# Optimization experiments

Measured on AMD Instinct MI355X. Metric: run time of the kernel, lower is better.

## Reference

```python
import jax, jax.numpy as jnp
import numpy as np
import math

B, T, C, H, L, V = 16, 512, 1024, 16, 4, 32000
D = C // H


def setup_inputs() -> dict:
    key = jax.random.key(0)
    ks = jax.random.split(key, 10)
    X = jax.random.randint(ks[0], (B, T), 0, V)
    S = jax.random.bernoulli(ks[1], 0.5, (B, T)).astype(jnp.int32)
    # I + S must equal 1 everywhere, else get_attn_mask fully masks a row -> NaN softmax
    I = (1 - S).astype(jnp.float32)
    s = 0.02
    emb_table = jax.random.normal(ks[2], (V + 1, C), jnp.float32) * s
    pos_emb = jax.random.normal(ks[3], (T, C), jnp.float32) * s
    qkv_w = jax.random.normal(ks[4], (L, 3 * C, C), jnp.float32) * s
    out_w = jax.random.normal(ks[5], (L, C, C), jnp.float32) * s
    ffn_w1 = jax.random.normal(ks[6], (L, C, C), jnp.float32) * s
    ffn_b1 = jnp.zeros((L, C), jnp.float32)
    ffn_w2 = jax.random.normal(ks[7], (L, C, C), jnp.float32) * s
    ffn_b2 = jnp.zeros((L, C), jnp.float32)
    return dict(X=X, I=I, S=S, emb_table=emb_table, pos_emb=pos_emb,
                qkv_w=qkv_w, out_w=out_w, ffn_w1=ffn_w1, ffn_b1=ffn_b1,
                ffn_w2=ffn_w2, ffn_b2=ffn_b2)


def _forward(X, I, S, emb_table, pos_emb, qkv_w, out_w, ffn_w1, ffn_b1, ffn_w2, ffn_b2):
    # token_to_embeddings: unobserved (S==0) tokens remapped to sentinel index V
    Xm = X * S + (1 - S) * V                      # [B,T]
    x = emb_table[Xm] + pos_emb[None]             # [B,T,C]
    # additive mask from outer product of validity flags m = I + S
    m = I + S.astype(I.dtype)                     # [B,T]
    prod = m[:, :, None] * m[:, None, :]          # [B,T,T]
    bias = jnp.where(prod == 1.0, 0.0, -jnp.inf)[:, None]  # [B,1,T,T]
    scale = 1.0 / math.sqrt(D)
    for i in range(L):
        wq, wk, wv = qkv_w[i, :C], qkv_w[i, C:2 * C], qkv_w[i, 2 * C:]
        q = (x @ wq.T).reshape(B, T, H, D)
        k = (x @ wk.T).reshape(B, T, H, D)
        v = (x @ wv.T).reshape(B, T, H, D)
        scores = jnp.einsum('bqhd,bkhd->bhqk', q * scale, k) + bias
        attn = jax.nn.softmax(scores, axis=-1)
        o = jnp.einsum('bhqk,bkhd->bqhd', attn, v).reshape(B, T, C)
        x = o @ out_w[i].T + x                    # out projection + residual
        h = jax.nn.relu(x @ ffn_w1[i].T + ffn_b1[i])
        x = x + (h @ ffn_w2[i].T + ffn_b2[i])
    # readout: bmm(x^T, I) -> [B,C]
    return jnp.einsum('btc,bt->bc', x, I)


def reference(X, I, S, emb_table, pos_emb, qkv_w, out_w, ffn_w1, ffn_b1, ffn_w2, ffn_b2):
    return _forward(X, I, S, emb_table, pos_emb, qkv_w, out_w,
                    ffn_w1, ffn_b1, ffn_w2, ffn_b2)
```

## Files before the change

kernel.cpp:

```cpp
#include <hip/hip_runtime.h>
#include <stdint.h>

#define LAYERS 4
#define BB 16
#define TT 512
#define CC 1024
#define HH 16
#define DD 64
#define VV 32000
#define MM (BB*TT)

typedef __attribute__((ext_vector_type(8))) short bf16x8;
typedef __attribute__((ext_vector_type(4))) float f32x4;
typedef __attribute__((ext_vector_type(16))) float f32x16;

__device__ __forceinline__ unsigned short f2b(float f) {
  union { float f; unsigned int u; } v; v.f = f;
  unsigned int r = v.u + 0x7FFFu + ((v.u >> 16) & 1u);
  return (unsigned short)(r >> 16);
}
__device__ __forceinline__ float blo(unsigned int u) {
  union { unsigned int x; float f; } v; v.x = u << 16; return v.f;
}
__device__ __forceinline__ float bhi(unsigned int u) {
  union { unsigned int x; float f; } v; v.x = u & 0xFFFF0000u; return v.f;
}
__device__ __forceinline__ uint32_t pkbf(float lo, float hi) {
  uint32_t d; asm("v_cvt_pk_bf16_f32 %0, %1, %2" : "=v"(d) : "v"(lo), "v"(hi)); return d;
}
__device__ __forceinline__ float ex2(float x) {
  float r; asm("v_exp_f32 %0, %1" : "=v"(r) : "v"(x)); return r;
}
__device__ __forceinline__ void gload16(const unsigned short* g, const unsigned short* lds) {
  __builtin_amdgcn_global_load_lds((const __attribute__((address_space(1))) void*)g,
                                   (__attribute__((address_space(3))) void*)lds, 16, 0, 0);
}

__global__ __launch_bounds__(256) void cvt_kernel(const float* __restrict__ src,
                                                  unsigned short* __restrict__ dst, int n4) {
  int i = blockIdx.x * 256 + threadIdx.x;
  if (i >= n4) return;
  float4 v = ((const float4*)src)[i];
  ushort4 o; o.x = f2b(v.x); o.y = f2b(v.y); o.z = f2b(v.z); o.w = f2b(v.w);
  ((ushort4*)dst)[i] = o;
}

__global__ __launch_bounds__(256) void embed_kernel(const int* __restrict__ X, const int* __restrict__ S,
    const float* __restrict__ emb, const float* __restrict__ pos,
    float* __restrict__ x, unsigned short* __restrict__ xb) {
  int bt = blockIdx.x; int tid = threadIdx.x;
  int t = bt & (TT - 1);
  int tok = S[bt] ? X[bt] : VV;
  float4 e = ((const float4*)(emb + (size_t)tok * CC))[tid];
  float4 p = ((const float4*)(pos + (size_t)t * CC))[tid];
  float4 r; r.x = e.x + p.x; r.y = e.y + p.y; r.z = e.z + p.z; r.w = e.w + p.w;
  ((float4*)(x + (size_t)bt * CC))[tid] = r;
  ushort4 ub; ub.x = f2b(r.x); ub.y = f2b(r.y); ub.z = f2b(r.z); ub.w = f2b(r.w);
  ((ushort4*)(xb + (size_t)bt * CC))[tid] = ub;
}

template<int EPI>
__global__ __launch_bounds__(512, 1) void gemm4_kernel(
    const unsigned short* __restrict__ A,
    const unsigned short* __restrict__ W,
    float* __restrict__ xres,
    unsigned short* __restrict__ outb,
    const float* __restrict__ bias,
    int N, int nbx) {
  extern __shared__ unsigned short lds[];
  const int K = 1024;
  const int tid = threadIdx.x;
  const int wv = tid >> 6, ln = tid & 63;
  const int g = ln >> 4, rr = ln & 15;
  const int wm = wv >> 1, wn = wv & 1;

  const int nwg = gridDim.x;
  const int bid = blockIdx.x;
  const int swz = (bid & 7) * (nwg >> 3) + (bid >> 3);
  const int by = swz / nbx, bx = swz - by * nbx;
  const int brow = by * 256, bcol = bx * 128;

  const unsigned short* asrc[4];
  const unsigned short* bsrc[2];
  #pragma unroll
  for (int rd = 0; rd < 4; ++rd) {
    int ch = rd * 512 + tid;
    int row = ch >> 3, c = (ch & 7) ^ (row & 7);
    asrc[rd] = A + (size_t)(brow + row) * K + c * 8;
  }
  #pragma unroll
  for (int rd = 0; rd < 2; ++rd) {
    int ch = rd * 512 + tid;
    int row = ch >> 3, c = (ch & 7) ^ (row & 7);
    bsrc[rd] = W + (size_t)(bcol + row) * K + c * 8;
  }

  auto stage = [&](int tile, int buf) {
    unsigned short* Ad = lds + buf * 24576 + wv * 512;
    unsigned short* Bd = lds + buf * 24576 + 16384 + wv * 512;
    int ko = tile * 64;
    #pragma unroll
    for (int rd = 0; rd < 4; ++rd) gload16(asrc[rd] + ko, Ad + rd * 4096);
    #pragma unroll
    for (int rd = 0; rd < 2; ++rd) gload16(bsrc[rd] + ko, Bd + rd * 4096);
  };

  f32x4 acc[4][4];
  #pragma unroll
  for (int i = 0; i < 4; ++i)
    #pragma unroll
    for (int j = 0; j < 4; ++j)
      acc[i][j] = (f32x4){0.f, 0.f, 0.f, 0.f};

  stage(0, 0);
  stage(1, 1);

  int bufc = 0;
  for (int t = 0; t < 16; ++t) {
    int bufn = bufc + 2; if (bufn >= 3) bufn -= 3;
    if (t < 14) {
      stage(t + 2, bufn);
      asm volatile("s_waitcnt vmcnt(12)" ::: "memory");
    } else if (t == 14) {
      asm volatile("s_waitcnt vmcnt(6)" ::: "memory");
    } else {
      asm volatile("s_waitcnt vmcnt(0)" ::: "memory");
    }
    __builtin_amdgcn_s_barrier();
    __builtin_amdgcn_sched_barrier(0);

    const unsigned short* Ab = lds + bufc * 24576;
    const unsigned short* Bb = Ab + 16384;
    bf16x8 av[2][4], bv[2][4];
    #pragma unroll
    for (int kk = 0; kk < 2; ++kk) {
      int chx = ((kk * 4 + g) ^ (rr & 7)) << 3;
      #pragma unroll
      for (int i = 0; i < 4; ++i) {
        av[kk][i] = *(const bf16x8*)(Ab + (wm * 64 + i * 16 + rr) * 64 + chx);
        bv[kk][i] = *(const bf16x8*)(Bb + (wn * 64 + i * 16 + rr) * 64 + chx);
      }
    }
    __builtin_amdgcn_s_setprio(1);
    #pragma unroll
    for (int kk = 0; kk < 2; ++kk)
      #pragma unroll
      for (int i = 0; i < 4; ++i)
        #pragma unroll
        for (int j = 0; j < 4; ++j)
          acc[i][j] = __builtin_amdgcn_mfma_f32_16x16x32_bf16(av[kk][i], bv[kk][j], acc[i][j], 0, 0, 0);
    __builtin_amdgcn_s_setprio(0);
    __builtin_amdgcn_sched_barrier(0);
    __builtin_amdgcn_s_barrier();
    bufc += 1; if (bufc == 3) bufc = 0;
  }

  #pragma unroll
  for (int i = 0; i < 4; ++i) {
    #pragma unroll
    for (int j = 0; j < 4; ++j) {
      #pragma unroll
      for (int q = 0; q < 4; ++q) {
        int rowg = brow + wm * 64 + i * 16 + g * 4 + q;
        int colg = bcol + wn * 64 + j * 16 + rr;
        size_t off = (size_t)rowg * N + colg;
        float vacc = acc[i][j][q];
        if (EPI == 0) {
          outb[off] = f2b(vacc);
        } else if (EPI == 1) {
          float nx = xres[off] + vacc;
          xres[off] = nx; outb[off] = f2b(nx);
        } else if (EPI == 2) {
          float hv = vacc + bias[colg];
          hv = hv > 0.f ? hv : 0.f;
          outb[off] = f2b(hv);
        } else {
          float nx = xres[off] + vacc + bias[colg];
          xres[off] = nx; outb[off] = f2b(nx);
        }
      }
    }
  }
}

template<int E>
__device__ __forceinline__ bf16x8 buildP(const f32x16& p) {
  uint32_t a = pkbf(p[E + 0], p[E + 1]);
  uint32_t b = pkbf(p[E + 4], p[E + 5]);
  uint32_t c = pkbf(p[E + 2], p[E + 3]);
  uint32_t d = pkbf(p[E + 6], p[E + 7]);
  asm("v_permlane32_swap_b32 %0, %1" : "+v"(a), "+v"(b));
  asm("v_permlane32_swap_b32 %0, %1" : "+v"(c), "+v"(d));
  union { uint32_t u[4]; bf16x8 v; } r;
  r.u[0] = a; r.u[1] = c; r.u[2] = b; r.u[3] = d;
  return r.v;
}

__global__ __launch_bounds__(256) void attn_kernel(const unsigned short* __restrict__ qkv,
                                                   unsigned short* __restrict__ ob) {
  __shared__ unsigned short Kl[64 * 64];
  __shared__ unsigned short Vt[64 * 64];
  const int tid = threadIdx.x;
  const int wv = tid >> 6, ln = tid & 63;
  const int lq = ln & 31, hi = ln >> 5;
  const int qt = blockIdx.x >> 8, bh = blockIdx.x & 255;
  const int b = bh >> 4, h = bh & 15;
  const int qrow = qt * 128 + wv * 32 + lq;
  const size_t rowQ = (size_t)(b * TT + qrow) * 3072 + h * 64;

  const float cs = 0.125f * 1.44269504f;
  bf16x8 qf[4];
  #pragma unroll
  for (int t = 0; t < 4; ++t) {
    uint4 u = *(const uint4*)(qkv + rowQ + t * 16 + hi * 8);
    uint32_t w[4] = {u.x, u.y, u.z, u.w};
    union { uint32_t u4[4]; bf16x8 v; } cv;
    #pragma unroll
    for (int j = 0; j < 4; ++j) cv.u4[j] = pkbf(blo(w[j]) * cs, bhi(w[j]) * cs);
    qf[t] = cv.v;
  }

  f32x16 o0 = {}, o1 = {};
  float mrun = -3.0e38f, lsum = 0.f;

  for (int kv0 = 0; kv0 < TT; kv0 += 64) {
    if (kv0) __syncthreads();
    #pragma unroll
    for (int r = 0; r < 2; ++r) {
      int ch = r * 256 + tid;
      int k = ch >> 3, cc = ch & 7;
      int sg = (k & 7) ^ (k >> 3);
      const unsigned short* gs = qkv + (size_t)(b * TT + kv0 + k) * 3072 + 1024 + h * 64 + ((cc ^ sg) << 3);
      gload16(gs, Kl + (size_t)(r * 256 + wv * 64) * 8);
    }
    {
      int cc = tid & 7, kp = tid >> 3;
      int k = kp * 2;
      const unsigned short* gv = qkv + (size_t)(b * TT + kv0 + k) * 3072 + 2048 + h * 64 + cc * 8;
      uint4 g1 = *(const uint4*)gv;
      uint4 g2 = *(const uint4*)(gv + 3072);
      uint32_t w1[4] = {g1.x, g1.y, g1.z, g1.w}, w2[4] = {g2.x, g2.y, g2.z, g2.w};
      #pragma unroll
      for (int j = 0; j < 8; ++j) {
        int d = cc * 8 + j;
        uint32_t dw = (j & 1) ? ((w1[j >> 1] >> 16) | (w2[j >> 1] & 0xFFFF0000u))
                              : ((w1[j >> 1] & 0xFFFFu) | (w2[j >> 1] << 16));
        int sg = (d & 7) ^ (d >> 3);
        *(uint32_t*)(Vt + d * 64 + (k ^ (sg << 3))) = dw;
      }
    }
    __syncthreads();

    f32x16 s0 = {}, s1 = {};
    #pragma unroll
    for (int t = 0; t < 4; ++t) {
      int r0 = lq, r1 = 32 + lq;
      bf16x8 a0 = *(const bf16x8*)(Kl + r0 * 64 + ((((t << 1) | hi) ^ ((r0 & 7) ^ (r0 >> 3))) << 3));
      bf16x8 a1 = *(const bf16x8*)(Kl + r1 * 64 + ((((t << 1) | hi) ^ ((r1 & 7) ^ (r1 >> 3))) << 3));
      s0 = __builtin_amdgcn_mfma_f32_32x32x16_bf16(a0, qf[t], s0, 0, 0, 0);
      s1 = __builtin_amdgcn_mfma_f32_32x32x16_bf16(a1, qf[t], s1, 0, 0, 0);
    }

    float mx = s0[0];
    #pragma unroll
    for (int r = 1; r < 16; ++r) mx = fmaxf(mx, s0[r]);
    #pragma unroll
    for (int r = 0; r < 16; ++r) mx = fmaxf(mx, s1[r]);
    mx = fmaxf(mx, __shfl_xor(mx, 32));
    float mnew = fmaxf(mrun, mx);
    float cf = ex2(mrun - mnew);
    mrun = mnew;
    lsum *= cf;
    #pragma unroll
    for (int r = 0; r < 16; ++r) { o0[r] *= cf; o1[r] *= cf; }
    #pragma unroll
    for (int r = 0; r < 16; ++r) {
      s0[r] = ex2(s0[r] - mnew);
      s1[r] = ex2(s1[r] - mnew);
      lsum += s0[r] + s1[r];
    }

    bf16x8 pf0 = buildP<0>(s0);
    bf16x8 pf1 = buildP<8>(s0);
    bf16x8 pf2 = buildP<0>(s1);
    bf16x8 pf3 = buildP<8>(s1);

    #pragma unroll
    for (int t = 0; t < 4; ++t) {
      bf16x8 pf = (t == 0) ? pf0 : (t == 1) ? pf1 : (t == 2) ? pf2 : pf3;
      int d0 = lq, d1 = 32 + lq;
      bf16x8 v0 = *(const bf16x8*)(Vt + d0 * 64 + ((((t << 1) | hi) ^ ((d0 & 7) ^ (d0 >> 3))) << 3));
      bf16x8 v1 = *(const bf16x8*)(Vt + d1 * 64 + ((((t << 1) | hi) ^ ((d1 & 7) ^ (d1 >> 3))) << 3));
      o0 = __builtin_amdgcn_mfma_f32_32x32x16_bf16(v0, pf, o0, 0, 0, 0);
      o1 = __builtin_amdgcn_mfma_f32_32x32x16_bf16(v1, pf, o1, 0, 0, 0);
    }
  }

  lsum += __shfl_xor(lsum, 32);
  float inv = 1.f / lsum;
  size_t orow = (size_t)(b * TT + qrow) * CC + h * 64;
  #pragma unroll
  for (int md = 0; md < 2; ++md) {
    #pragma unroll
    for (int rq = 0; rq < 4; ++rq) {
      int d0 = md * 32 + rq * 8 + hi * 4;
      float e0 = (md ? o1[rq * 4 + 0] : o0[rq * 4 + 0]) * inv;
      float e1 = (md ? o1[rq * 4 + 1] : o0[rq * 4 + 1]) * inv;
      float e2 = (md ? o1[rq * 4 + 2] : o0[rq * 4 + 2]) * inv;
      float e3 = (md ? o1[rq * 4 + 3] : o0[rq * 4 + 3]) * inv;
      uint2 st; st.x = pkbf(e0, e1); st.y = pkbf(e2, e3);
      *(uint2*)(ob + orow + d0) = st;
    }
  }
}

__global__ __launch_bounds__(256) void final_kernel(const float* __restrict__ x,
                                                    const float* __restrict__ I,
                                                    float* __restrict__ out) {
  int b = blockIdx.x >> 2;
  int c = ((blockIdx.x & 3) << 8) + threadIdx.x;
  float acc = 0.f;
  const float* xp = x + (size_t)b * TT * CC + c;
  const float* Ip = I + (size_t)b * TT;
  for (int t = 0; t < TT; ++t) acc = fmaf(xp[(size_t)t * CC], Ip[t], acc);
  out[b * CC + c] = acc;
}

extern "C" void kernel_launch(void* const* d_in, const int* in_sizes, int n_in,
                              void* d_out, int out_size, void* d_ws, size_t ws_size,
                              hipStream_t stream) {
  const int*   X      = (const int*)d_in[0];
  const float* I      = (const float*)d_in[1];
  const int*   S      = (const int*)d_in[2];
  const float* emb    = (const float*)d_in[3];
  const float* pos    = (const float*)d_in[4];
  const float* qkv_w  = (const float*)d_in[5];
  const float* out_w  = (const float*)d_in[6];
  const float* ffn_w1 = (const float*)d_in[7];
  const float* ffn_b1 = (const float*)d_in[8];
  const float* ffn_w2 = (const float*)d_in[9];
  const float* ffn_b2 = (const float*)d_in[10];
  float* out = (float*)d_out;

  char* ws = (char*)d_ws;
  size_t off = 0;
  auto walloc = [&](size_t bytes) { char* p = ws + off; off += (bytes + 255) & ~(size_t)255; return p; };
  unsigned short* wqkv = (unsigned short*)walloc((size_t)LAYERS * 3 * CC * CC * 2);
  unsigned short* wo   = (unsigned short*)walloc((size_t)LAYERS * CC * CC * 2);
  unsigned short* w1   = (unsigned short*)walloc((size_t)LAYERS * CC * CC * 2);
  unsigned short* w2   = (unsigned short*)walloc((size_t)LAYERS * CC * CC * 2);
  float*          x    = (float*)walloc((size_t)MM * CC * 4);
  unsigned short* xb   = (unsigned short*)walloc((size_t)MM * CC * 2);
  unsigned short* qkvb = (unsigned short*)walloc((size_t)MM * 3 * CC * 2);
  unsigned short* obuf = (unsigned short*)walloc((size_t)MM * CC * 2);
  unsigned short* hbuf = (unsigned short*)walloc((size_t)MM * CC * 2);
  if (off > ws_size) return;

  int n4;
  n4 = LAYERS * 3 * CC * CC / 4; cvt_kernel<<<(n4 + 255) / 256, 256, 0, stream>>>(qkv_w, wqkv, n4);
  n4 = LAYERS * CC * CC / 4;     cvt_kernel<<<(n4 + 255) / 256, 256, 0, stream>>>(out_w, wo, n4);
  n4 = LAYERS * CC * CC / 4;     cvt_kernel<<<(n4 + 255) / 256, 256, 0, stream>>>(ffn_w1, w1, n4);
  n4 = LAYERS * CC * CC / 4;     cvt_kernel<<<(n4 + 255) / 256, 256, 0, stream>>>(ffn_w2, w2, n4);

  embed_kernel<<<MM, 256, 0, stream>>>(X, S, emb, pos, x, xb);

  const size_t ldsB = 144 * 1024;
  for (int l = 0; l < LAYERS; ++l) {
    gemm4_kernel<0><<<(MM / 256) * (3 * CC / 128), 512, ldsB, stream>>>(
        xb, wqkv + (size_t)l * 3 * CC * CC, nullptr, qkvb, nullptr, 3 * CC, 3 * CC / 128);
    attn_kernel<<<4 * 256, 256, 0, stream>>>(qkvb, obuf);
    gemm4_kernel<1><<<(MM / 256) * (CC / 128), 512, ldsB, stream>>>(
        obuf, wo + (size_t)l * CC * CC, x, xb, nullptr, CC, CC / 128);
    gemm4_kernel<2><<<(MM / 256) * (CC / 128), 512, ldsB, stream>>>(
        xb, w1 + (size_t)l * CC * CC, nullptr, hbuf, ffn_b1 + l * CC, CC, CC / 128);
    gemm4_kernel<3><<<(MM / 256) * (CC / 128), 512, ldsB, stream>>>(
        hbuf, w2 + (size_t)l * CC * CC, x, xb, ffn_b2 + l * CC, CC, CC / 128);
  }

  final_kernel<<<BB * 4, 256, 0, stream>>>(x, I, out);
}
```

Baseline: 823.7 us.

## Split GEMM k-tile into two half-steps interleaving A/B prefetch with MFMA

Restructures the GEMM main loop so each 64-wide k tile is processed in two 32-wide halves. The A-tile global-to-LDS prefetch is issued in the first half and the B-tile prefetch in the second, each after that half's LDS fragment reads. The aim is to spread global load issue across the MFMA work and keep fewer fragment registers live. The cost is an extra barrier per k tile and changed waitcnt accounting, which could stall if the counts are off.

New measurement: 791.4 us. 1.04x faster.

```diff
diff --git a/kernel.cpp b/kernel.cpp
--- a/kernel.cpp
+++ b/kernel.cpp
@@ -60,7 +60,7 @@
 }
 
 template<int EPI>
-__global__ __launch_bounds__(512, 1) void gemm4_kernel(
+__global__ __launch_bounds__(512, 1) void gemm5_kernel(
     const unsigned short* __restrict__ A,
     const unsigned short* __restrict__ W,
     float* __restrict__ xres,
@@ -95,13 +95,16 @@
     bsrc[rd] = W + (size_t)(bcol + row) * K + c * 8;
   }
 
-  auto stage = [&](int tile, int buf) {
+  auto stageA = [&](int tile, int buf) {
     unsigned short* Ad = lds + buf * 24576 + wv * 512;
+    int ko = tile * 64;
+    #pragma unroll
+    for (int rd = 0; rd < 4; ++rd) gload16(asrc[rd] + ko, Ad + rd * 4096);
+  };
+  auto stageB = [&](int tile, int buf) {
     unsigned short* Bd = lds + buf * 24576 + 16384 + wv * 512;
     int ko = tile * 64;
     #pragma unroll
-    for (int rd = 0; rd < 4; ++rd) gload16(asrc[rd] + ko, Ad + rd * 4096);
-    #pragma unroll
     for (int rd = 0; rd < 2; ++rd) gload16(bsrc[rd] + ko, Bd + rd * 4096);
   };
 
@@ -112,46 +115,64 @@
     for (int j = 0; j < 4; ++j)
       acc[i][j] = (f32x4){0.f, 0.f, 0.f, 0.f};
 
-  stage(0, 0);
-  stage(1, 1);
+  stageA(0, 0); stageB(0, 0);
+  stageA(1, 1); stageB(1, 1);
+  asm volatile("s_waitcnt vmcnt(6)" ::: "memory");
+  __builtin_amdgcn_s_barrier();
 
   int bufc = 0;
   for (int t = 0; t < 16; ++t) {
     int bufn = bufc + 2; if (bufn >= 3) bufn -= 3;
-    if (t < 14) {
-      stage(t + 2, bufn);
-      asm volatile("s_waitcnt vmcnt(12)" ::: "memory");
-    } else if (t == 14) {
-      asm volatile("s_waitcnt vmcnt(6)" ::: "memory");
-    } else {
-      asm volatile("s_waitcnt vmcnt(0)" ::: "memory");
-    }
-    __builtin_amdgcn_s_barrier();
-    __builtin_amdgcn_sched_barrier(0);
-
     const unsigned short* Ab = lds + bufc * 24576;
     const unsigned short* Bb = Ab + 16384;
-    bf16x8 av[2][4], bv[2][4];
-    #pragma unroll
-    for (int kk = 0; kk < 2; ++kk) {
-      int chx = ((kk * 4 + g) ^ (rr & 7)) << 3;
-      #pragma unroll
-      for (int i = 0; i < 4; ++i) {
-        av[kk][i] = *(const bf16x8*)(Ab + (wm * 64 + i * 16 + rr) * 64 + chx);
-        bv[kk][i] = *(const bf16x8*)(Bb + (wn * 64 + i * 16 + rr) * 64 + chx);
-      }
-    }
-    __builtin_amdgcn_s_setprio(1);
-    #pragma unroll
-    for (int kk = 0; kk < 2; ++kk)
+
+    {
+      bf16x8 av[4], bv[4];
+      const int chx = ((0 * 4 + g) ^ (rr & 7)) << 3;
+      #pragma unroll
+      for (int i = 0; i < 4; ++i)
+        av[i] = *(const bf16x8*)(Ab + (wm * 64 + i * 16 + rr) * 64 + chx);
+      #pragma unroll
+      for (int j = 0; j < 4; ++j)
+        bv[j] = *(const bf16x8*)(Bb + (wn * 64 + j * 16 + rr) * 64 + chx);
+      if (t < 14) stageA(t + 2, bufn);
+      __builtin_amdgcn_sched_barrier(0);
+      __builtin_amdgcn_s_barrier();
+      __builtin_amdgcn_s_setprio(1);
       #pragma unroll
       for (int i = 0; i < 4; ++i)
         #pragma unroll
         for (int j = 0; j < 4; ++j)
-          acc[i][j] = __builtin_amdgcn_mfma_f32_16x16x32_bf16(av[kk][i], bv[kk][j], acc[i][j], 0, 0, 0);
-    __builtin_amdgcn_s_setprio(0);
-    __builtin_amdgcn_sched_barrier(0);
-    __builtin_amdgcn_s_barrier();
+          acc[i][j] = __builtin_amdgcn_mfma_f32_16x16x32_bf16(av[i], bv[j], acc[i][j], 0, 0, 0);
+      __builtin_amdgcn_s_setprio(0);
+      __builtin_amdgcn_sched_barrier(0);
+      __builtin_amdgcn_s_barrier();
+    }
+
+    {
+      bf16x8 av[4], bv[4];
+      const int chx = ((1 * 4 + g) ^ (rr & 7)) << 3;
+      #pragma unroll
+      for (int i = 0; i < 4; ++i)
+        av[i] = *(const bf16x8*)(Ab + (wm * 64 + i * 16 + rr) * 64 + chx);
+      #pragma unroll
+      for (int j = 0; j < 4; ++j)
+        bv[j] = *(const bf16x8*)(Bb + (wn * 64 + j * 16 + rr) * 64 + chx);
+      if (t < 14) stageB(t + 2, bufn);
+      __builtin_amdgcn_sched_barrier(0);
+      __builtin_amdgcn_s_barrier();
+      __builtin_amdgcn_s_setprio(1);
+      #pragma unroll
+      for (int i = 0; i < 4; ++i)
+        #pragma unroll
+        for (int j = 0; j < 4; ++j)
+          acc[i][j] = __builtin_amdgcn_mfma_f32_16x16x32_bf16(av[i], bv[j], acc[i][j], 0, 0, 0);
+      __builtin_amdgcn_s_setprio(0);
+      if (t < 14) { asm volatile("s_waitcnt vmcnt(6)" ::: "memory"); }
+      else if (t == 14) { asm volatile("s_waitcnt vmcnt(0)" ::: "memory"); }
+      __builtin_amdgcn_sched_barrier(0);
+      __builtin_amdgcn_s_barrier();
+    }
     bufc += 1; if (bufc == 3) bufc = 0;
   }
 
@@ -366,14 +387,14 @@
 
   const size_t ldsB = 144 * 1024;
   for (int l = 0; l < LAYERS; ++l) {
-    gemm4_kernel<0><<<(MM / 256) * (3 * CC / 128), 512, ldsB, stream>>>(
+    gemm5_kernel<0><<<(MM / 256) * (3 * CC / 128), 512, ldsB, stream>>>(
         xb, wqkv + (size_t)l * 3 * CC * CC, nullptr, qkvb, nullptr, 3 * CC, 3 * CC / 128);
     attn_kernel<<<4 * 256, 256, 0, stream>>>(qkvb, obuf);
-    gemm4_kernel<1><<<(MM / 256) * (CC / 128), 512, ldsB, stream>>>(
+    gemm5_kernel<1><<<(MM / 256) * (CC / 128), 512, ldsB, stream>>>(
         obuf, wo + (size_t)l * CC * CC, x, xb, nullptr, CC, CC / 128);
-    gemm4_kernel<2><<<(MM / 256) * (CC / 128), 512, ldsB, stream>>>(
+    gemm5_kernel<2><<<(MM / 256) * (CC / 128), 512, ldsB, stream>>>(
         xb, w1 + (size_t)l * CC * CC, nullptr, hbuf, ffn_b1 + l * CC, CC, CC / 128);
-    gemm4_kernel<3><<<(MM / 256) * (CC / 128), 512, ldsB, stream>>>(
+    gemm5_kernel<3><<<(MM / 256) * (CC / 128), 512, ldsB, stream>>>(
         hbuf, w2 + (size_t)l * CC * CC, x, xb, ffn_b2 + l * CC, CC, CC / 128);
   }
 
```

## Restructure GEMM to 256 threads, 2 blocks/CU, BK=32 with larger per-wave tiles

Applied to the files above, without the earlier changes.

The GEMM kernel moves from 512 threads with one block per CU to 256 threads with two blocks per CU. The K-tile drops from 64 to 32 (32 iterations), each wave now computes a 128x64 output tile with 8x4 accumulators, and LDS per block is halved so two blocks can share a CU. The aim is better latency hiding through two co-resident blocks and more MFMA work per LDS fragment load. The XOR swizzle on the LDS layout is removed, which may bring back bank conflicts, and the larger accumulator set raises register pressure.

After: 926.4 us. 12.5% more time.

```diff
diff --git a/kernel.cpp b/kernel.cpp
--- a/kernel.cpp
+++ b/kernel.cpp
@@ -60,7 +60,7 @@
 }
 
 template<int EPI>
-__global__ __launch_bounds__(512, 1) void gemm4_kernel(
+__global__ __launch_bounds__(256, 2) void gemm6_kernel(
     const unsigned short* __restrict__ A,
     const unsigned short* __restrict__ W,
     float* __restrict__ xres,
@@ -83,45 +83,41 @@
   const unsigned short* asrc[4];
   const unsigned short* bsrc[2];
   #pragma unroll
-  for (int rd = 0; rd < 4; ++rd) {
-    int ch = rd * 512 + tid;
-    int row = ch >> 3, c = (ch & 7) ^ (row & 7);
-    asrc[rd] = A + (size_t)(brow + row) * K + c * 8;
-  }
-  #pragma unroll
-  for (int rd = 0; rd < 2; ++rd) {
-    int ch = rd * 512 + tid;
-    int row = ch >> 3, c = (ch & 7) ^ (row & 7);
-    bsrc[rd] = W + (size_t)(bcol + row) * K + c * 8;
-  }
+  for (int rd = 0; rd < 4; ++rd)
+    asrc[rd] = A + (size_t)(brow + rd * 64 + (tid >> 2)) * K + (tid & 3) * 8;
+  #pragma unroll
+  for (int rd = 0; rd < 2; ++rd)
+    bsrc[rd] = W + (size_t)(bcol + rd * 64 + (tid >> 2)) * K + (tid & 3) * 8;
 
   auto stage = [&](int tile, int buf) {
-    unsigned short* Ad = lds + buf * 24576 + wv * 512;
-    unsigned short* Bd = lds + buf * 24576 + 16384 + wv * 512;
-    int ko = tile * 64;
-    #pragma unroll
-    for (int rd = 0; rd < 4; ++rd) gload16(asrc[rd] + ko, Ad + rd * 4096);
-    #pragma unroll
-    for (int rd = 0; rd < 2; ++rd) gload16(bsrc[rd] + ko, Bd + rd * 4096);
+    unsigned short* Ad = lds + buf * 12288 + wv * 512;
+    unsigned short* Bd = lds + buf * 12288 + 8192 + wv * 512;
+    int ko = tile * 32;
+    #pragma unroll
+    for (int rd = 0; rd < 4; ++rd) gload16(asrc[rd] + ko, Ad + rd * 2048);
+    #pragma unroll
+    for (int rd = 0; rd < 2; ++rd) gload16(bsrc[rd] + ko, Bd + rd * 2048);
   };
 
-  f32x4 acc[4][4];
-  #pragma unroll
-  for (int i = 0; i < 4; ++i)
+  f32x4 acc[8][4];
+  #pragma unroll
+  for (int i = 0; i < 8; ++i)
     #pragma unroll
     for (int j = 0; j < 4; ++j)
       acc[i][j] = (f32x4){0.f, 0.f, 0.f, 0.f};
 
   stage(0, 0);
   stage(1, 1);
+  asm volatile("s_waitcnt vmcnt(6)" ::: "memory");
+  __builtin_amdgcn_s_barrier();
 
   int bufc = 0;
-  for (int t = 0; t < 16; ++t) {
+  for (int t = 0; t < 32; ++t) {
     int bufn = bufc + 2; if (bufn >= 3) bufn -= 3;
-    if (t < 14) {
+    if (t < 30) {
       stage(t + 2, bufn);
       asm volatile("s_waitcnt vmcnt(12)" ::: "memory");
-    } else if (t == 14) {
+    } else if (t == 30) {
       asm volatile("s_waitcnt vmcnt(6)" ::: "memory");
     } else {
       asm volatile("s_waitcnt vmcnt(0)" ::: "memory");
@@ -129,26 +125,22 @@
     __builtin_amdgcn_s_barrier();
     __builtin_amdgcn_sched_barrier(0);
 
-    const unsigned short* Ab = lds + bufc * 24576;
-    const unsigned short* Bb = Ab + 16384;
-    bf16x8 av[2][4], bv[2][4];
-    #pragma unroll
-    for (int kk = 0; kk < 2; ++kk) {
-      int chx = ((kk * 4 + g) ^ (rr & 7)) << 3;
+    const unsigned short* Ab = lds + bufc * 12288;
+    const unsigned short* Bb = Ab + 8192;
+    bf16x8 av[8], bv[4];
+    #pragma unroll
+    for (int i = 0; i < 8; ++i)
+      av[i] = *(const bf16x8*)(Ab + (wm * 128 + i * 16 + rr) * 32 + g * 8);
+    #pragma unroll
+    for (int j = 0; j < 4; ++j)
+      bv[j] = *(const bf16x8*)(Bb + (wn * 64 + j * 16 + rr) * 32 + g * 8);
+
+    __builtin_amdgcn_s_setprio(1);
+    #pragma unroll
+    for (int i = 0; i < 8; ++i)
       #pragma unroll
-      for (int i = 0; i < 4; ++i) {
-        av[kk][i] = *(const bf16x8*)(Ab + (wm * 64 + i * 16 + rr) * 64 + chx);
-        bv[kk][i] = *(const bf16x8*)(Bb + (wn * 64 + i * 16 + rr) * 64 + chx);
-      }
-    }
-    __builtin_amdgcn_s_setprio(1);
-    #pragma unroll
-    for (int kk = 0; kk < 2; ++kk)
-      #pragma unroll
-      for (int i = 0; i < 4; ++i)
-        #pragma unroll
-        for (int j = 0; j < 4; ++j)
-          acc[i][j] = __builtin_amdgcn_mfma_f32_16x16x32_bf16(av[kk][i], bv[kk][j], acc[i][j], 0, 0, 0);
+      for (int j = 0; j < 4; ++j)
+        acc[i][j] = __builtin_amdgcn_mfma_f32_16x16x32_bf16(av[i], bv[j], acc[i][j], 0, 0, 0);
     __builtin_amdgcn_s_setprio(0);
     __builtin_amdgcn_sched_barrier(0);
     __builtin_amdgcn_s_barrier();
@@ -156,12 +148,12 @@
   }
 
   #pragma unroll
-  for (int i = 0; i < 4; ++i) {
+  for (int i = 0; i < 8; ++i) {
     #pragma unroll
     for (int j = 0; j < 4; ++j) {
       #pragma unroll
       for (int q = 0; q < 4; ++q) {
-        int rowg = brow + wm * 64 + i * 16 + g * 4 + q;
+        int rowg = brow + wm * 128 + i * 16 + g * 4 + q;
         int colg = bcol + wn * 64 + j * 16 + rr;
         size_t off = (size_t)rowg * N + colg;
         float vacc = acc[i][j][q];
@@ -364,16 +356,16 @@
 
   embed_kernel<<<MM, 256, 0, stream>>>(X, S, emb, pos, x, xb);
 
-  const size_t ldsB = 144 * 1024;
+  const size_t ldsB = 72 * 1024;
   for (int l = 0; l < LAYERS; ++l) {
-    gemm4_kernel<0><<<(MM / 256) * (3 * CC / 128), 512, ldsB, stream>>>(
+    gemm6_kernel<0><<<(MM / 256) * (3 * CC / 128), 256, ldsB, stream>>>(
         xb, wqkv + (size_t)l * 3 * CC * CC, nullptr, qkvb, nullptr, 3 * CC, 3 * CC / 128);
     attn_kernel<<<4 * 256, 256, 0, stream>>>(qkvb, obuf);
-    gemm4_kernel<1><<<(MM / 256) * (CC / 128), 512, ldsB, stream>>>(
+    gemm6_kernel<1><<<(MM / 256) * (CC / 128), 256, ldsB, stream>>>(
         obuf, wo + (size_t)l * CC * CC, x, xb, nullptr, CC, CC / 128);
-    gemm4_kernel<2><<<(MM / 256) * (CC / 128), 512, ldsB, stream>>>(
+    gemm6_kernel<2><<<(MM / 256) * (CC / 128), 256, ldsB, stream>>>(
         xb, w1 + (size_t)l * CC * CC, nullptr, hbuf, ffn_b1 + l * CC, CC, CC / 128);
-    gemm4_kernel<3><<<(MM / 256) * (CC / 128), 512, ldsB, stream>>>(
+    gemm6_kernel<3><<<(MM / 256) * (CC / 128), 256, ldsB, stream>>>(
         hbuf, w2 + (size_t)l * CC * CC, x, xb, ffn_b2 + l * CC, CC, CC / 128);
   }
 
```

## Use 4-wave GEMM with larger per-wave tiles and double-buffer attention K/V

Applied to the files above, without the earlier changes.

The GEMM now runs with 256 threads instead of 512, so each wave computes a 128x64 sub-tile. Each wave issues twice as many global-to-LDS loads, and the vmcnt waits are adjusted to match. The attention kernel gets double-buffered K and V^T tiles in shared memory: the next tile's K is staged and V is prefetched into registers while the current tile is computed. This replaces one of the two syncthreads per iteration with a single barrier, aiming to hide load latency. The trade-off is higher register pressure (32 accumulators per wave in the GEMM) and fewer waves available to hide latency.

Measured after the change: 934.0 us. +13.4%, slower.

```diff
diff --git a/kernel.cpp b/kernel.cpp
--- a/kernel.cpp
+++ b/kernel.cpp
@@ -60,7 +60,7 @@
 }
 
 template<int EPI>
-__global__ __launch_bounds__(512, 1) void gemm4_kernel(
+__global__ __launch_bounds__(256, 1) void gemm7_kernel(
     const unsigned short* __restrict__ A,
     const unsigned short* __restrict__ W,
     float* __restrict__ xres,
@@ -80,18 +80,18 @@
   const int by = swz / nbx, bx = swz - by * nbx;
   const int brow = by * 256, bcol = bx * 128;
 
-  const unsigned short* asrc[4];
-  const unsigned short* bsrc[2];
+  const unsigned short* asrc[8];
+  const unsigned short* bsrc[4];
+  #pragma unroll
+  for (int rd = 0; rd < 8; ++rd) {
+    int row = rd * 32 + (tid >> 3);
+    int c = (tid & 7) ^ (row & 7);
+    asrc[rd] = A + (size_t)(brow + row) * K + c * 8;
+  }
   #pragma unroll
   for (int rd = 0; rd < 4; ++rd) {
-    int ch = rd * 512 + tid;
-    int row = ch >> 3, c = (ch & 7) ^ (row & 7);
-    asrc[rd] = A + (size_t)(brow + row) * K + c * 8;
-  }
-  #pragma unroll
-  for (int rd = 0; rd < 2; ++rd) {
-    int ch = rd * 512 + tid;
-    int row = ch >> 3, c = (ch & 7) ^ (row & 7);
+    int row = rd * 32 + (tid >> 3);
+    int c = (tid & 7) ^ (row & 7);
     bsrc[rd] = W + (size_t)(bcol + row) * K + c * 8;
   }
 
@@ -100,29 +100,31 @@
     unsigned short* Bd = lds + buf * 24576 + 16384 + wv * 512;
     int ko = tile * 64;
     #pragma unroll
-    for (int rd = 0; rd < 4; ++rd) gload16(asrc[rd] + ko, Ad + rd * 4096);
-    #pragma unroll
-    for (int rd = 0; rd < 2; ++rd) gload16(bsrc[rd] + ko, Bd + rd * 4096);
+    for (int rd = 0; rd < 8; ++rd) gload16(asrc[rd] + ko, Ad + rd * 2048);
+    #pragma unroll
+    for (int rd = 0; rd < 4; ++rd) gload16(bsrc[rd] + ko, Bd + rd * 2048);
   };
 
-  f32x4 acc[4][4];
-  #pragma unroll
-  for (int i = 0; i < 4; ++i)
+  f32x4 acc[8][4];
+  #pragma unroll
+  for (int i = 0; i < 8; ++i)
     #pragma unroll
     for (int j = 0; j < 4; ++j)
       acc[i][j] = (f32x4){0.f, 0.f, 0.f, 0.f};
 
   stage(0, 0);
   stage(1, 1);
+  asm volatile("s_waitcnt vmcnt(12)" ::: "memory");
+  __builtin_amdgcn_s_barrier();
 
   int bufc = 0;
   for (int t = 0; t < 16; ++t) {
     int bufn = bufc + 2; if (bufn >= 3) bufn -= 3;
     if (t < 14) {
       stage(t + 2, bufn);
+      asm volatile("s_waitcnt vmcnt(24)" ::: "memory");
+    } else if (t == 14) {
       asm volatile("s_waitcnt vmcnt(12)" ::: "memory");
-    } else if (t == 14) {
-      asm volatile("s_waitcnt vmcnt(6)" ::: "memory");
     } else {
       asm volatile("s_waitcnt vmcnt(0)" ::: "memory");
     }
@@ -131,37 +133,36 @@
 
     const unsigned short* Ab = lds + bufc * 24576;
     const unsigned short* Bb = Ab + 16384;
-    bf16x8 av[2][4], bv[2][4];
     #pragma unroll
     for (int kk = 0; kk < 2; ++kk) {
-      int chx = ((kk * 4 + g) ^ (rr & 7)) << 3;
+      const int chx = ((kk * 4 + g) ^ (rr & 7)) << 3;
+      bf16x8 av[8], bv[4];
       #pragma unroll
-      for (int i = 0; i < 4; ++i) {
-        av[kk][i] = *(const bf16x8*)(Ab + (wm * 64 + i * 16 + rr) * 64 + chx);
-        bv[kk][i] = *(const bf16x8*)(Bb + (wn * 64 + i * 16 + rr) * 64 + chx);
-      }
-    }
-    __builtin_amdgcn_s_setprio(1);
-    #pragma unroll
-    for (int kk = 0; kk < 2; ++kk)
+      for (int i = 0; i < 8; ++i)
+        av[i] = *(const bf16x8*)(Ab + (wm * 128 + i * 16 + rr) * 64 + chx);
       #pragma unroll
-      for (int i = 0; i < 4; ++i)
+      for (int j = 0; j < 4; ++j)
+        bv[j] = *(const bf16x8*)(Bb + (wn * 64 + j * 16 + rr) * 64 + chx);
+      __builtin_amdgcn_s_setprio(1);
+      #pragma unroll
+      for (int i = 0; i < 8; ++i)
         #pragma unroll
         for (int j = 0; j < 4; ++j)
-          acc[i][j] = __builtin_amdgcn_mfma_f32_16x16x32_bf16(av[kk][i], bv[kk][j], acc[i][j], 0, 0, 0);
-    __builtin_amdgcn_s_setprio(0);
+          acc[i][j] = __builtin_amdgcn_mfma_f32_16x16x32_bf16(av[i], bv[j], acc[i][j], 0, 0, 0);
+      __builtin_amdgcn_s_setprio(0);
+    }
     __builtin_amdgcn_sched_barrier(0);
     __builtin_amdgcn_s_barrier();
     bufc += 1; if (bufc == 3) bufc = 0;
   }
 
   #pragma unroll
-  for (int i = 0; i < 4; ++i) {
+  for (int i = 0; i < 8; ++i) {
     #pragma unroll
     for (int j = 0; j < 4; ++j) {
       #pragma unroll
       for (int q = 0; q < 4; ++q) {
-        int rowg = brow + wm * 64 + i * 16 + g * 4 + q;
+        int rowg = brow + wm * 128 + i * 16 + g * 4 + q;
         int colg = bcol + wn * 64 + j * 16 + rr;
         size_t off = (size_t)rowg * N + colg;
         float vacc = acc[i][j][q];
@@ -198,8 +199,8 @@
 
 __global__ __launch_bounds__(256) void attn_kernel(const unsigned short* __restrict__ qkv,
                                                    unsigned short* __restrict__ ob) {
-  __shared__ unsigned short Kl[64 * 64];
-  __shared__ unsigned short Vt[64 * 64];
+  __shared__ unsigned short Kl[2][64 * 64];
+  __shared__ unsigned short Vt[2][64 * 64];
   const int tid = threadIdx.x;
   const int wv = tid >> 6, ln = tid & 63;
   const int lq = ln & 31, hi = ln >> 5;
@@ -220,43 +221,55 @@
     qf[t] = cv.v;
   }
 
-  f32x16 o0 = {}, o1 = {};
-  float mrun = -3.0e38f, lsum = 0.f;
-
-  for (int kv0 = 0; kv0 < TT; kv0 += 64) {
-    if (kv0) __syncthreads();
+  auto stageK = [&](int i, int p) {
     #pragma unroll
     for (int r = 0; r < 2; ++r) {
       int ch = r * 256 + tid;
       int k = ch >> 3, cc = ch & 7;
       int sg = (k & 7) ^ (k >> 3);
-      const unsigned short* gs = qkv + (size_t)(b * TT + kv0 + k) * 3072 + 1024 + h * 64 + ((cc ^ sg) << 3);
-      gload16(gs, Kl + (size_t)(r * 256 + wv * 64) * 8);
-    }
-    {
-      int cc = tid & 7, kp = tid >> 3;
-      int k = kp * 2;
-      const unsigned short* gv = qkv + (size_t)(b * TT + kv0 + k) * 3072 + 2048 + h * 64 + cc * 8;
-      uint4 g1 = *(const uint4*)gv;
-      uint4 g2 = *(const uint4*)(gv + 3072);
-      uint32_t w1[4] = {g1.x, g1.y, g1.z, g1.w}, w2[4] = {g2.x, g2.y, g2.z, g2.w};
-      #pragma unroll
-      for (int j = 0; j < 8; ++j) {
-        int d = cc * 8 + j;
-        uint32_t dw = (j & 1) ? ((w1[j >> 1] >> 16) | (w2[j >> 1] & 0xFFFF0000u))
-                              : ((w1[j >> 1] & 0xFFFFu) | (w2[j >> 1] << 16));
-        int sg = (d & 7) ^ (d >> 3);
-        *(uint32_t*)(Vt + d * 64 + (k ^ (sg << 3))) = dw;
-      }
-    }
-    __syncthreads();
+      const unsigned short* gs = qkv + (size_t)(b * TT + i * 64 + k) * 3072 + 1024 + h * 64 + ((cc ^ sg) << 3);
+      gload16(gs, &Kl[p][(size_t)(r * 256 + wv * 64) * 8]);
+    }
+  };
+  auto loadV = [&](int i, uint4& g1, uint4& g2) {
+    int cc = tid & 7, kp = tid >> 3;
+    const unsigned short* gv = qkv + (size_t)(b * TT + i * 64 + kp * 2) * 3072 + 2048 + h * 64 + cc * 8;
+    g1 = *(const uint4*)gv;
+    g2 = *(const uint4*)(gv + 3072);
+  };
+  auto writeVt = [&](int p, uint4 g1, uint4 g2) {
+    int cc = tid & 7, k = (tid >> 3) * 2;
+    uint32_t w1[4] = {g1.x, g1.y, g1.z, g1.w}, w2[4] = {g2.x, g2.y, g2.z, g2.w};
+    #pragma unroll
+    for (int j = 0; j < 8; ++j) {
+      int d = cc * 8 + j;
+      uint32_t dw = (j & 1) ? ((w1[j >> 1] >> 16) | (w2[j >> 1] & 0xFFFF0000u))
+                            : ((w1[j >> 1] & 0xFFFFu) | (w2[j >> 1] << 16));
+      int sg = (d & 7) ^ (d >> 3);
+      *(uint32_t*)(&Vt[p][d * 64 + (k ^ (sg << 3))]) = dw;
+    }
+  };
+
+  f32x16 o0 = {}, o1 = {};
+  float mrun = -3.0e38f, lsum = 0.f;
+
+  uint4 vg1, vg2;
+  stageK(0, 0);
+  loadV(0, vg1, vg2);
+  writeVt(0, vg1, vg2);
+  asm volatile("s_waitcnt lgkmcnt(0)" ::: "memory");
+  __builtin_amdgcn_s_barrier();
+
+  for (int i = 0; i < 8; ++i) {
+    const int p = i & 1;
+    if (i < 7) { stageK(i + 1, p ^ 1); loadV(i + 1, vg1, vg2); }
 
     f32x16 s0 = {}, s1 = {};
     #pragma unroll
     for (int t = 0; t < 4; ++t) {
       int r0 = lq, r1 = 32 + lq;
-      bf16x8 a0 = *(const bf16x8*)(Kl + r0 * 64 + ((((t << 1) | hi) ^ ((r0 & 7) ^ (r0 >> 3))) << 3));
-      bf16x8 a1 = *(const bf16x8*)(Kl + r1 * 64 + ((((t << 1) | hi) ^ ((r1 & 7) ^ (r1 >> 3))) << 3));
+      bf16x8 a0 = *(const bf16x8*)(&Kl[p][r0 * 64 + ((((t << 1) | hi) ^ ((r0 & 7) ^ (r0 >> 3))) << 3)]);
+      bf16x8 a1 = *(const bf16x8*)(&Kl[p][r1 * 64 + ((((t << 1) | hi) ^ ((r1 & 7) ^ (r1 >> 3))) << 3)]);
       s0 = __builtin_amdgcn_mfma_f32_32x32x16_bf16(a0, qf[t], s0, 0, 0, 0);
       s1 = __builtin_amdgcn_mfma_f32_32x32x16_bf16(a1, qf[t], s1, 0, 0, 0);
     }
@@ -285,15 +298,21 @@
     bf16x8 pf2 = buildP<0>(s1);
     bf16x8 pf3 = buildP<8>(s1);
 
+    if (i < 7) writeVt(p ^ 1, vg1, vg2);
+
     #pragma unroll
     for (int t = 0; t < 4; ++t) {
       bf16x8 pf = (t == 0) ? pf0 : (t == 1) ? pf1 : (t == 2) ? pf2 : pf3;
       int d0 = lq, d1 = 32 + lq;
-      bf16x8 v0 = *(const bf16x8*)(Vt + d0 * 64 + ((((t << 1) | hi) ^ ((d0 & 7) ^ (d0 >> 3))) << 3));
-      bf16x8 v1 = *(const bf16x8*)(Vt + d1 * 64 + ((((t << 1) | hi) ^ ((d1 & 7) ^ (d1 >> 3))) << 3));
+      bf16x8 v0 = *(const bf16x8*)(&Vt[p][d0 * 64 + ((((t << 1) | hi) ^ ((d0 & 7) ^ (d0 >> 3))) << 3)]);
+      bf16x8 v1 = *(const bf16x8*)(&Vt[p][d1 * 64 + ((((t << 1) | hi) ^ ((d1 & 7) ^ (d1 >> 3))) << 3)]);
       o0 = __builtin_amdgcn_mfma_f32_32x32x16_bf16(v0, pf, o0, 0, 0, 0);
       o1 = __builtin_amdgcn_mfma_f32_32x32x16_bf16(v1, pf, o1, 0, 0, 0);
     }
+
+    asm volatile("s_waitcnt lgkmcnt(0)" ::: "memory");
+    __builtin_amdgcn_sched_barrier(0);
+    __builtin_amdgcn_s_barrier();
   }
 
   lsum += __shfl_xor(lsum, 32);
@@ -366,14 +385,14 @@
 
   const size_t ldsB = 144 * 1024;
   for (int l = 0; l < LAYERS; ++l) {
-    gemm4_kernel<0><<<(MM / 256) * (3 * CC / 128), 512, ldsB, stream>>>(
+    gemm7_kernel<0><<<(MM / 256) * (3 * CC / 128), 256, ldsB, stream>>>(
         xb, wqkv + (size_t)l * 3 * CC * CC, nullptr, qkvb, nullptr, 3 * CC, 3 * CC / 128);
     attn_kernel<<<4 * 256, 256, 0, stream>>>(qkvb, obuf);
-    gemm4_kernel<1><<<(MM / 256) * (CC / 128), 512, ldsB, stream>>>(
+    gemm7_kernel<1><<<(MM / 256) * (CC / 128), 256, ldsB, stream>>>(
         obuf, wo + (size_t)l * CC * CC, x, xb, nullptr, CC, CC / 128);
-    gemm4_kernel<2><<<(MM / 256) * (CC / 128), 512, ldsB, stream>>>(
+    gemm7_kernel<2><<<(MM / 256) * (CC / 128), 256, ldsB, stream>>>(
         xb, w1 + (size_t)l * CC * CC, nullptr, hbuf, ffn_b1 + l * CC, CC, CC / 128);
-    gemm4_kernel<3><<<(MM / 256) * (CC / 128), 512, ldsB, stream>>>(
+    gemm7_kernel<3><<<(MM / 256) * (CC / 128), 256, ldsB, stream>>>(
         hbuf, w2 + (size_t)l * CC * CC, x, xb, ffn_b2 + l * CC, CC, CC / 128);
   }
 
```
